# Kernel tuning notes

Hardware: AMD Instinct MI355X
Metric: run time of the kernel (lower is better)

Reference implementation:

```python
import jax, jax.numpy as jnp
import numpy as np

PI = float(np.pi)


def _conv2d(x, w, b, pad):
    out = jax.lax.conv_general_dilated(x, w, (1, 1), ((pad, pad), (pad, pad)),
                                       dimension_numbers=('NCHW', 'OIHW', 'NCHW'))
    return out + b[None, :, None, None]


def _group_norm(x, gamma, beta, groups, eps=1e-5):
    B, C, h, w = x.shape
    xg = x.reshape(B, groups, C // groups, h, w)
    mu = xg.mean(axis=(2, 3, 4), keepdims=True)
    var = xg.var(axis=(2, 3, 4), keepdims=True)
    xn = ((xg - mu) / jnp.sqrt(var + eps)).reshape(B, C, h, w)
    return xn * gamma[None, :, None, None] + beta[None, :, None, None]


def _l2n(x, eps=1e-12):
    return x / jnp.maximum(jnp.linalg.norm(x, axis=1, keepdims=True), eps)


def _dense_sift(x):
    # kornia DenseSIFTDescriptor defaults: 8 ang bins, 4x4 spatial bins,
    # spatial_bin_size=4, rootsift=True, clipval=0.2, stride=1, padding=1
    eps = 1e-10
    NA = 8
    # 'diff' spatial gradient with replicate padding, normalized (/2)
    xp = jnp.pad(x, ((0, 0), (0, 0), (1, 1), (1, 1)), mode='edge')
    gx = (xp[:, :, 1:-1, 2:] - xp[:, :, 1:-1, :-2]) * 0.5
    gy = (xp[:, :, 2:, 1:-1] - xp[:, :, :-2, 1:-1]) * 0.5
    mag = jnp.sqrt(gx * gx + gy * gy + eps)[:, 0]           # [B,H,W]
    ori = jnp.arctan2(gy, gx + eps)[:, 0] + 2.0 * PI
    o_big = NA * ori / (2.0 * PI)
    bo0f = jnp.floor(o_big)
    wo1_ = o_big - bo0f
    wo0 = (1.0 - wo1_) * mag
    wo1 = wo1_ * mag
    bo0 = bo0f.astype(jnp.int32) % NA
    bo1 = (bo0 + 1) % NA
    bins = jnp.arange(NA).reshape(1, NA, 1, 1)
    ang = ((bo0[:, None] == bins).astype(x.dtype) * wo0[:, None]
           + (bo1[:, None] == bins).astype(x.dtype) * wo1[:, None])  # [B,8,H,W]
    # SIFT pooling kernel ksize=4 (triangle weights), conv pad=2 -> H+1,W+1
    xc2 = np.array([0.5, 1.5, 1.5, 0.5], np.float32)
    pool1 = np.outer(xc2, xc2) / 4.0
    pk = jnp.asarray(np.tile(pool1[None, None], (NA, 1, 1, 1)))  # depthwise [8,1,4,4]
    pooled = jax.lax.conv_general_dilated(ang, pk, (1, 1), ((2, 2), (2, 2)),
                dimension_numbers=('NCHW', 'OIHW', 'NCHW'), feature_group_count=NA)
    # identity reshape conv: 128 = 8 ang * 4*4 spatial bins, pad=1 -> back to H,W
    rk = jnp.asarray(np.eye(128, dtype=np.float32).reshape(128, NA, 4, 4))
    out = jax.lax.conv_general_dilated(pooled, rk, (1, 1), ((1, 1), (1, 1)),
                dimension_numbers=('NCHW', 'OIHW', 'NCHW'))
    out = jnp.clip(_l2n(out), 0.0, 0.2)
    out = _l2n(out)
    l1 = jnp.maximum(jnp.sum(jnp.abs(out), axis=1, keepdims=True), 1e-12)
    return jnp.sqrt(out / l1 + eps)  # rootsift


def _joint_bilateral(x, guide, ksize=5, sigma_color=0.1, sigma_space=1.5):
    pad = ksize // 2
    ax = np.arange(ksize, dtype=np.float32) - ksize // 2
    g1 = np.exp(-ax ** 2 / (2.0 * sigma_space ** 2))
    g1 = g1 / g1.sum()
    sk = np.outer(g1, g1)  # normalized 5x5 gaussian space kernel
    xp = jnp.pad(x, ((0, 0), (0, 0), (pad, pad), (pad, pad)), mode='reflect')
    gp = jnp.pad(guide, ((0, 0), (0, 0), (pad, pad), (pad, pad)), mode='reflect')
    h, w = x.shape[2], x.shape[3]
    inv = -0.5 / (sigma_color ** 2)
    num = jnp.zeros_like(x)
    den = jnp.zeros((x.shape[0], 1, h, w), x.dtype)
    for dy in range(ksize):           # fixed 5x5 tap loop, accumulated in-place
        for dx in range(ksize):
            gs = gp[:, :, dy:dy + h, dx:dx + w]
            cd = jnp.sum(jnp.abs(gs - guide), axis=1, keepdims=True) ** 2  # l1 squared
            wgt = sk[dy, dx] * jnp.exp(inv * cd)
            num = num + wgt * xp[:, :, dy:dy + h, dx:dx + w]
            den = den + wgt
    return num / den


def _forward(x, gt, w1, b1, g1w, g1b, w2, b2, g2w, g2b, w3, b3, g3w, g3b,
             w4, b4, g4w, g4b, w5, b5):
    orig = x
    f = _dense_sift(x)
    f = jax.nn.relu(_group_norm(_conv2d(f, w1, b1, 2), g1w, g1b, 8))
    f = jax.nn.relu(_group_norm(_conv2d(f, w2, b2, 1), g2w, g2b, 8))
    f = jax.nn.relu(_group_norm(_conv2d(f, w3, b3, 1), g3w, g3b, 4))
    f = jax.nn.relu(_group_norm(_conv2d(f, w4, b4, 1), g4w, g4b, 4))
    f = _conv2d(f, w5, b5, 1)
    # rgb_to_yuv(gt)[:, 1:] as guidance
    r, g, b = gt[:, 0], gt[:, 1], gt[:, 2]
    u = -0.147 * r - 0.289 * g + 0.436 * b
    v = 0.615 * r - 0.515 * g - 0.100 * b
    guide = jnp.stack([u, v], axis=1)
    f = _joint_bilateral(f, guide)

    def _rescale(c, lo, hi):
        c = (c - c.min()) / (c.max() - c.min() + 1e-6)  # global min/max over B,H,W
        c = jnp.clip(c, 0.0, 1.0)
        return c * (hi - lo) + lo

    U = _rescale(f[:, 0], -0.436, 0.436)
    V = _rescale(f[:, 1], -0.615, 0.615)
    Y = orig[:, 0]
    R = Y + 1.14 * V
    G = Y - 0.396 * U - 0.581 * V
    B = Y + 2.029 * U
    return jnp.stack([R, G, B], axis=1)


def setup_inputs() -> dict:
    key = jax.random.key(0)
    ks = jax.random.split(key, 16)
    B = 4
    d = {
        'x': jax.random.uniform(ks[0], (B, 1, 270, 512), jnp.float32),
        'gt': jax.random.uniform(ks[1], (B, 3, 270, 512), jnp.float32),
        'w1': jax.random.normal(ks[2], (64, 128, 5, 5), jnp.float32) * 0.02,
        'b1': jnp.zeros((64,), jnp.float32),
        'g1w': jnp.ones((64,), jnp.float32), 'g1b': jnp.zeros((64,), jnp.float32),
        'w2': jax.random.normal(ks[3], (32, 64, 3, 3), jnp.float32) * 0.04,
        'b2': jnp.zeros((32,), jnp.float32),
        'g2w': jnp.ones((32,), jnp.float32), 'g2b': jnp.zeros((32,), jnp.float32),
        'w3': jax.random.normal(ks[4], (16, 32, 3, 3), jnp.float32) * 0.05,
        'b3': jnp.zeros((16,), jnp.float32),
        'g3w': jnp.ones((16,), jnp.float32), 'g3b': jnp.zeros((16,), jnp.float32),
        'w4': jax.random.normal(ks[5], (8, 16, 3, 3), jnp.float32) * 0.08,
        'b4': jnp.zeros((8,), jnp.float32),
        'g4w': jnp.ones((8,), jnp.float32), 'g4b': jnp.zeros((8,), jnp.float32),
        'w5': jax.random.normal(ks[6], (2, 8, 3, 3), jnp.float32) * 0.1,
        'b5': jnp.zeros((2,), jnp.float32),
    }
    return d


def reference(x, gt, w1, b1, g1w, g1b, w2, b2, g2w, g2b, w3, b3, g3w, g3b,
              w4, b4, g4w, g4b, w5, b5):
    return _forward(x, gt, w1, b1, g1w, g1b, w2, b2, g2w, g2b, w3, b3, g3w, g3b,
                    w4, b4, g4w, g4b, w5, b5)
```

## Files before the change

kernel.cpp:

```cpp
#include <hip/hip_runtime.h>

constexpr int NB  = 4;
constexpr int IH  = 270;
constexpr int IW  = 512;
constexpr int NPIX = IH * IW;
constexpr int PH  = 271;
constexpr int PW  = 513;
constexpr float TWO_PI_F = 6.28318530717958647692f;

typedef short  bf16x8 __attribute__((ext_vector_type(8)));
typedef float floatx4 __attribute__((ext_vector_type(4)));

__device__ inline short f2bf(float x) {
  union { float f; unsigned u; } un; un.f = x;
  unsigned r = un.u + 0x7fff + ((un.u >> 16) & 1);
  return (short)(r >> 16);
}
__device__ inline unsigned fkey(float f) {
  unsigned u = __float_as_uint(f);
  return (u & 0x80000000u) ? ~u : (u | 0x80000000u);
}
__device__ inline float funkey(unsigned k) {
  unsigned u = (k & 0x80000000u) ? (k ^ 0x80000000u) : ~k;
  return __uint_as_float(u);
}
__device__ inline void gn_coef_thread(const float* __restrict__ stats,
                                      const float* __restrict__ gamma,
                                      const float* __restrict__ beta,
                                      float* cA, float* cB, int C, int chper, int b) {
  int c = threadIdx.x;
  if (c < C) {
    int g0 = (c / chper) * chper;
    float S = 0.f, S2 = 0.f;
    for (int k = 0; k < chper; k++) {
      S  += stats[(b * C + g0 + k) * 2];
      S2 += stats[(b * C + g0 + k) * 2 + 1];
    }
    double Nd = (double)chper * NPIX;
    double mu = (double)S / Nd;
    double var = (double)S2 / Nd - mu * mu;
    double rstd = 1.0 / sqrt(var + 1e-5);
    float A = (float)rstd * gamma[c];
    cA[c] = A;
    cB[c] = beta[c] - (float)mu * A;
  }
}

__device__ inline void mfma_pack_one(const float* __restrict__ w, short* __restrict__ wB,
                                     int i, int CO, int CI, int KK, int CHUNKS) {
  int j = i & 7, l = (i >> 3) & 63, f = i >> 9;
  int t = f % KK; int fc = f / KK; int cc = fc % CHUNKS; int g = fc / CHUNKS;
  int ci = cc * 32 + ((l >> 4) << 3) + j;
  int co = g * 16 + (l & 15);
  float v = (ci < CI && co < CO) ? w[((size_t)co * CI + ci) * KK + t] : 0.f;
  wB[i] = f2bf(v);
}
__device__ inline void repack_one(const float* __restrict__ w, float* __restrict__ wT,
                                  int i, int CO, int CI, int KK) {
  int o = i / (CI * KK);
  int r = i % (CI * KK);
  int ci = r / KK, kk = r % KK;
  wT[(kk * CI + ci) * CO + o] = w[i];
}
__global__ __launch_bounds__(256) void prep_kernel(
    const float* __restrict__ w1, const float* __restrict__ w2,
    const float* __restrict__ w3, const float* __restrict__ w4,
    const float* __restrict__ w5,
    short* __restrict__ w1B, short* __restrict__ w2B, short* __restrict__ w3B,
    float* __restrict__ w4T, float* __restrict__ w5T) {
  constexpr int N1 = 4 * 4 * 25 * 512;
  constexpr int N2 = 2 * 2 * 9 * 512;
  constexpr int N3 = 1 * 1 * 9 * 512;
  constexpr int N4 = 8 * 16 * 9;
  constexpr int N5 = 2 * 8 * 9;
  int i = blockIdx.x * 256 + threadIdx.x;
  if (i < N1) { mfma_pack_one(w1, w1B, i, 64, 128, 25, 4); return; }
  i -= N1;
  if (i < N2) { mfma_pack_one(w2, w2B, i, 32, 64, 9, 2); return; }
  i -= N2;
  if (i < N3) { mfma_pack_one(w3, w3B, i, 16, 32, 9, 1); return; }
  i -= N3;
  if (i < N4) { repack_one(w4, w4T, i, 8, 16, 9); return; }
  i -= N4;
  if (i < N5) { repack_one(w5, w5T, i, 2, 8, 9); return; }
}

__global__ __launch_bounds__(256) void pooled_kernel(
    const float* __restrict__ x, float* __restrict__ pooled) {
  const int b = blockIdx.z;
  const int px0 = blockIdx.x * 16, py0 = blockIdx.y * 16;
  __shared__ float wo0s[19][19];
  __shared__ float wo1s[19][19];
  __shared__ int   bo0s[19][19];
  const float* xb = x + (size_t)b * NPIX;

  for (int t = threadIdx.x; t < 19 * 19; t += 256) {
    int r = t / 19, c = t % 19;
    int gy = py0 - 2 + r, gx = px0 - 2 + c;
    float w0 = 0.f, w1v = 0.f; int b0 = 0;
    if (gy >= 0 && gy < IH && gx >= 0 && gx < IW) {
      int xm = gx > 0 ? gx - 1 : 0, xp = gx < IW - 1 ? gx + 1 : IW - 1;
      int ym = gy > 0 ? gy - 1 : 0, yp = gy < IH - 1 ? gy + 1 : IH - 1;
      float gxv = (xb[gy * IW + xp] - xb[gy * IW + xm]) * 0.5f;
      float gyv = (xb[yp * IW + gx] - xb[ym * IW + gx]) * 0.5f;
      float mag = sqrtf(gxv * gxv + gyv * gyv + 1e-10f);
      float ori = atan2f(gyv, gxv + 1e-10f) + TWO_PI_F;
      float obig = ori * (8.0f / TWO_PI_F);
      float bf = floorf(obig);
      float w1_ = obig - bf;
      w0  = (1.0f - w1_) * mag;
      w1v = w1_ * mag;
      b0  = ((int)bf) & 7;
    }
    wo0s[r][c] = w0; wo1s[r][c] = w1v; bo0s[r][c] = b0;
  }
  __syncthreads();

  const int t = threadIdx.x;
  const int lx = t % 16, ly = t / 16;
  const int py = py0 + ly, px = px0 + lx;
  if (py >= PH || px >= PW) return;

  const float pwt[4] = {0.25f, 0.75f, 0.75f, 0.25f};
  float acc[8] = {0, 0, 0, 0, 0, 0, 0, 0};
  for (int i = 0; i < 4; i++) {
    for (int j = 0; j < 4; j++) {
      int r = ly + i, c = lx + j;
      float w0 = wo0s[r][c], w1v = wo1s[r][c];
      int b0 = bo0s[r][c];
      int b1i = (b0 + 1) & 7;
      float pw = pwt[i] * pwt[j];
      #pragma unroll
      for (int a = 0; a < 8; a++) {
        float add = (a == b0 ? w0 : 0.f) + (a == b1i ? w1v : 0.f);
        acc[a] = fmaf(pw, add, acc[a]);
      }
    }
  }
  float* pb = pooled + (size_t)b * 8 * PH * PW;
  #pragma unroll
  for (int a = 0; a < 8; a++) pb[((size_t)a * PH + py) * PW + px] = acc[a];
}

__global__ __launch_bounds__(256) void sift_scalars_kernel(
    const float* __restrict__ pooled, float* __restrict__ s1g) {
  const int b = blockIdx.z;
  const int x0 = blockIdx.x * 16, y0 = blockIdx.y * 16;
  __shared__ float pt[8][19][19];
  const float* pb = pooled + (size_t)b * 8 * PH * PW;
  for (int t = threadIdx.x; t < 8 * 19 * 19; t += 256) {
    int a = t / 361, rc = t % 361, r = rc / 19, c = rc % 19;
    int gy = y0 - 1 + r, gx = x0 - 1 + c;
    float v = 0.f;
    if (gy >= 0 && gy < PH && gx >= 0 && gx < PW) v = pb[((size_t)a * PH + gy) * PW + gx];
    pt[a][r][c] = v;
  }
  __syncthreads();
  const int t = threadIdx.x;
  const int lx = t % 16, ly = t / 16;
  const int y = y0 + ly, x = x0 + lx;
  if (y >= IH) return;

  float sum2 = 0.f;
  for (int c = 0; c < 128; c++) {
    int a = c >> 4, i = (c >> 2) & 3, j = c & 3;
    float p = pt[a][ly + i][lx + j];
    sum2 = fmaf(p, p, sum2);
  }
  float s1 = 1.0f / fmaxf(sqrtf(sum2), 1e-12f);
  float st2 = 0.f, st = 0.f;
  for (int c = 0; c < 128; c++) {
    int a = c >> 4, i = (c >> 2) & 3, j = c & 3;
    float p = pt[a][ly + i][lx + j];
    float tv = fminf(p * s1, 0.2f);
    st2 = fmaf(tv, tv, st2);
    st += tv;
  }
  float s2 = 1.0f / fmaxf(sqrtf(st2), 1e-12f);
  float l1 = fmaxf(s2 * st, 1e-12f);
  float g = s2 / l1;
  float* o = s1g + (size_t)b * 2 * NPIX;
  o[y * IW + x] = s1;
  o[NPIX + y * IW + x] = g;
}

__global__ __launch_bounds__(256, 2) void conv1_mfma_kernel(
    const float* __restrict__ pooled, const float* __restrict__ s1g,
    const short* __restrict__ w1B, const float* __restrict__ bias,
    float* __restrict__ out, float* __restrict__ stats) {
  const int b = blockIdx.z;
  const int x0 = blockIdx.x * 16, y0 = blockIdx.y * 16;
  __shared__ __align__(16) char smem_raw[39440];
  short* desc = (short*)smem_raw;
  float* sc   = (float*)(smem_raw + 32000);
  float* pt   = (float*)(smem_raw + 35208);
  float* cout = (float*)smem_raw;

  const int tid = threadIdx.x;
  const int wave = tid >> 6, lane = tid & 63;
  const int quad = lane >> 4, lm = lane & 15;

  const float* pb = pooled + (size_t)b * 8 * PH * PW;
  const float* sb = s1g + (size_t)b * 2 * NPIX;
  for (int t = tid; t < 400; t += 256) {
    int r = t / 20, c = t % 20;
    int gy = y0 - 2 + r, gx = x0 - 2 + c;
    float a0 = 0.f, a1 = 0.f;
    if (gy >= 0 && gy < IH && gx >= 0 && gx < IW) {
      a0 = sb[gy * IW + gx];
      a1 = sb[NPIX + gy * IW + gx];
    }
    sc[t] = a0; sc[400 + t] = a1;
  }
  for (int t = tid; t < 1058; t += 256) {
    int pl = t / 529, rc = t % 529, r = rc / 23, c = rc % 23;
    int gy = y0 - 3 + r, gx = x0 - 3 + c;
    float v = 0.f;
    if (gy >= 0 && gy < PH && gx >= 0 && gx < PW) v = pb[((size_t)pl * PH + gy) * PW + gx];
    pt[t] = v;
  }

  floatx4 acc[4][4];
  #pragma unroll
  for (int n = 0; n < 4; n++)
    #pragma unroll
    for (int i = 0; i < 4; i++) acc[n][i] = (floatx4){0.f, 0.f, 0.f, 0.f};

  for (int cc = 0; cc < 4; cc++) {
    __syncthreads();
    for (int v = tid; v < 3200; v += 256) {
      int pos = v % 400, cg = v / 400;
      int r = pos / 20, c = pos % 20;
      int gy = y0 - 2 + r, gx = x0 - 2 + c;
      bool ok = (gy >= 0 && gy < IH && gx >= 0 && gx < IW);
      int al = cg >> 2;
      int ii = cg & 3;
      float s1v = sc[pos], gv = sc[400 + pos];
      const float* prow = pt + al * 529 + (r + ii) * 23 + c;
      unsigned short o4[4];
      #pragma unroll
      for (int q = 0; q < 4; q++) {
        float p = prow[q];
        float val = ok ? sqrtf(fminf(p * s1v, 0.2f) * gv + 1e-10f) : 0.f;
        o4[q] = (unsigned short)f2bf(val);
      }
      uint2 pk;
      pk.x = (unsigned)o4[0] | ((unsigned)o4[1] << 16);
      pk.y = (unsigned)o4[2] | ((unsigned)o4[3] << 16);
      *(uint2*)(desc + pos * 40 + cg * 4) = pk;
    }
    __syncthreads();

    if (cc < 3) {
      for (int t = tid; t < 1058; t += 256) {
        int pl = t / 529, rc = t % 529, r = rc / 23, c = rc % 23;
        int gy = y0 - 3 + r, gx = x0 - 3 + c;
        float v = 0.f;
        if (gy >= 0 && gy < PH && gx >= 0 && gx < PW)
          v = pb[((size_t)(2 * (cc + 1) + pl) * PH + gy) * PW + gx];
        pt[t] = v;
      }
    }

    #pragma unroll
    for (int ky = 0; ky < 5; ky++) {
      #pragma unroll
      for (int kx = 0; kx < 5; kx++) {
        bf16x8 bfr[4];
        #pragma unroll
        for (int n = 0; n < 4; n++) {
          int f = (n * 4 + cc) * 25 + ky * 5 + kx;
          bfr[n] = *(const bf16x8*)(w1B + ((size_t)f << 9) + (lane << 3));
        }
        bf16x8 av[4];
        #pragma unroll
        for (int i = 0; i < 4; i++) {
          int mt = wave * 4 + i;
          av[i] = *(const bf16x8*)(desc + ((mt + ky) * 20 + lm + kx) * 40 + quad * 8);
        }
        #pragma unroll
        for (int n = 0; n < 4; n++)
          #pragma unroll
          for (int i = 0; i < 4; i++)
            acc[n][i] = __builtin_amdgcn_mfma_f32_16x16x32_bf16(av[i], bfr[n], acc[n][i], 0, 0, 0);
      }
    }
  }

  float* ob = out + (size_t)b * 64 * NPIX;
  for (int h = 0; h < 2; h++) {
    __syncthreads();
    #pragma unroll
    for (int nn = 0; nn < 2; nn++)
      #pragma unroll
      for (int i = 0; i < 4; i++)
        #pragma unroll
        for (int r = 0; r < 4; r++)
          cout[(nn * 16 + lm) * 261 + (wave * 4 + i) * 16 + quad * 4 + r] = acc[h * 2 + nn][i][r];
    __syncthreads();
    for (int v = tid; v < 8192; v += 256) {
      int col = v >> 8, px = v & 255;
      int y = y0 + (px >> 4), x = x0 + (px & 15);
      if (y < IH)
        ob[(size_t)(h * 32 + col) * NPIX + y * IW + x] = cout[col * 261 + px] + bias[h * 32 + col];
    }
    int col = tid >> 3, seg = tid & 7;
    int co = h * 32 + col;
    float bv = bias[co];
    float sum = 0.f, sq = 0.f;
    #pragma unroll
    for (int rr = 0; rr < 2; rr++) {
      int row = seg * 2 + rr;
      if (y0 + row < IH) {
        #pragma unroll
        for (int k = 0; k < 16; k++) {
          float vv = cout[col * 261 + row * 16 + k] + bv;
          sum += vv; sq += vv * vv;
        }
      }
    }
    sum += __shfl_down(sum, 4); sq += __shfl_down(sq, 4);
    sum += __shfl_down(sum, 2); sq += __shfl_down(sq, 2);
    sum += __shfl_down(sum, 1); sq += __shfl_down(sq, 1);
    if ((tid & 7) == 0) {
      atomicAdd(&stats[(b * 64 + co) * 2], sum);
      atomicAdd(&stats[(b * 64 + co) * 2 + 1], sq);
    }
  }
}

template <int CI, int CO, int CHPER, bool STATS>
__global__ __launch_bounds__(256) void convk3_mfma_kernel(
    const float* __restrict__ xin, const short* __restrict__ wB,
    const float* __restrict__ bias, const float* __restrict__ statsIn,
    const float* __restrict__ gamma, const float* __restrict__ beta,
    float* __restrict__ statsOut, float* __restrict__ out) {
  constexpr int CHUNKS = CI / 32;
  constexpr int G = CO / 16;
  constexpr int MPW = 2 * G;
  constexpr int CIS = CI + 8;
  constexpr int TILE_B = 180 * CIS * 2;
  constexpr int COUT_B = CO * 133 * 4;
  constexpr int UNION_B = TILE_B > COUT_B ? TILE_B : COUT_B;
  __shared__ __align__(16) char sm[UNION_B + CI * 8];
  short* tile = (short*)sm;
  float* cout = (float*)sm;
  float* cA = (float*)(sm + UNION_B);
  float* cB = cA + CI;

  const int b = blockIdx.z;
  const int x0 = blockIdx.x * 16, y0 = blockIdx.y * 8;
  const int tid = threadIdx.x;
  const int wave = tid >> 6, lane = tid & 63;
  const int quad = lane >> 4, lm = lane & 15;
  const int n = wave % G, mh = wave / G;

  gn_coef_thread(statsIn, gamma, beta, cA, cB, CI, CHPER, b);
  __syncthreads();

  const float* xb = xin + (size_t)b * CI * NPIX;
  for (int v = tid; v < (CI / 2) * 180; v += 256) {
    int cp = v / 180, pos = v % 180;
    int r = pos / 18, c = pos % 18;
    int gy = y0 - 1 + r, gx = x0 - 1 + c;
    float v0 = 0.f, v1 = 0.f;
    if (gy >= 0 && gy < IH && gx >= 0 && gx < IW) {
      v0 = fmaxf(fmaf(xb[(size_t)(2 * cp) * NPIX + gy * IW + gx], cA[2 * cp], cB[2 * cp]), 0.f);
      v1 = fmaxf(fmaf(xb[(size_t)(2 * cp + 1) * NPIX + gy * IW + gx], cA[2 * cp + 1], cB[2 * cp + 1]), 0.f);
    }
    unsigned pk = (unsigned)(unsigned short)f2bf(v0) |
                  ((unsigned)(unsigned short)f2bf(v1) << 16);
    *(unsigned*)(tile + pos * CIS + 2 * cp) = pk;
  }
  __syncthreads();

  floatx4 acc[MPW];
  #pragma unroll
  for (int i = 0; i < MPW; i++) acc[i] = (floatx4){0.f, 0.f, 0.f, 0.f};

  #pragma unroll
  for (int cc = 0; cc < CHUNKS; cc++) {
    #pragma unroll
    for (int ky = 0; ky < 3; ky++) {
      #pragma unroll
      for (int kx = 0; kx < 3; kx++) {
        int f = (n * CHUNKS + cc) * 9 + ky * 3 + kx;
        bf16x8 bfr = *(const bf16x8*)(wB + ((size_t)f << 9) + (lane << 3));
        #pragma unroll
        for (int i = 0; i < MPW; i++) {
          int mt = mh * MPW + i;
          bf16x8 av = *(const bf16x8*)(tile + ((mt + ky) * 18 + lm + kx) * CIS + cc * 32 + quad * 8);
          acc[i] = __builtin_amdgcn_mfma_f32_16x16x32_bf16(av, bfr, acc[i], 0, 0, 0);
        }
      }
    }
  }
  __syncthreads();
  #pragma unroll
  for (int i = 0; i < MPW; i++) {
    #pragma unroll
    for (int r = 0; r < 4; r++) {
      int pixel = (mh * MPW + i) * 16 + quad * 4 + r;
      cout[(n * 16 + lm) * 133 + pixel] = acc[i][r];
    }
  }
  __syncthreads();
  float* ob = out + (size_t)b * CO * NPIX;
  for (int v = tid; v < CO * 128; v += 256) {
    int co = v >> 7, px = v & 127;
    int y = y0 + (px >> 4), x = x0 + (px & 15);
    if (y < IH) ob[(size_t)co * NPIX + y * IW + x] = cout[co * 133 + px] + bias[co];
  }
  if (STATS) {
    constexpr int TPC = 256 / CO;
    constexpr int PXT = 128 / TPC;
    int col = tid / TPC, seg = tid % TPC;
    float bv = bias[col];
    float sum = 0.f, sq = 0.f;
    #pragma unroll
    for (int k = 0; k < PXT; k++) {
      int p = seg * PXT + k;
      if (y0 + (p >> 4) < IH) {
        float vv = cout[col * 133 + p] + bv;
        sum += vv; sq += vv * vv;
      }
    }
    #pragma unroll
    for (int off = TPC / 2; off > 0; off >>= 1) {
      sum += __shfl_down(sum, off);
      sq  += __shfl_down(sq, off);
    }
    if (seg == 0) {
      atomicAdd(&statsOut[(b * CO + col) * 2], sum);
      atomicAdd(&statsOut[(b * CO + col) * 2 + 1], sq);
    }
  }
}

template <int CI, int CO, int CHPER, bool STATS>
__global__ __launch_bounds__(256) void convs_kernel(
    const float* __restrict__ xin, const float* __restrict__ wT,
    const float* __restrict__ bias, const float* __restrict__ statsIn,
    const float* __restrict__ gamma, const float* __restrict__ beta,
    float* __restrict__ statsOut, float* __restrict__ out) {
  constexpr int OPT = CO / 2;
  const int b = blockIdx.z;
  const int x0 = blockIdx.x * 16, y0 = blockIdx.y * 8;
  __shared__ float tile[CI * 180];
  __shared__ float cA[CI], cB[CI];
  __shared__ float ssum[CO], ssq[CO];
  gn_coef_thread(statsIn, gamma, beta, cA, cB, CI, CHPER, b);
  if (STATS && threadIdx.x < CO) { ssum[threadIdx.x] = 0.f; ssq[threadIdx.x] = 0.f; }
  __syncthreads();
  const float* xb = xin + (size_t)b * CI * NPIX;
  for (int t = threadIdx.x; t < CI * 180; t += 256) {
    int ci = t / 180, rc = t % 180, r = rc / 18, c = rc % 18;
    int gy = y0 - 1 + r, gx = x0 - 1 + c;
    float v = 0.f;
    if (gy >= 0 && gy < IH && gx >= 0 && gx < IW)
      v = fmaxf(fmaf(xb[(size_t)ci * NPIX + gy * IW + gx], cA[ci], cB[ci]), 0.f);
    tile[t] = v;
  }
  __syncthreads();
  const int t = threadIdx.x;
  const int px = t & 127, og = t >> 7;
  const int pyy = px >> 4, pxx = px & 15;
  const int oc0 = og * OPT;
  const int y = y0 + pyy, x = x0 + pxx;
  float acc[OPT] = {};
  for (int ky = 0; ky < 3; ky++) {
    for (int kx = 0; kx < 3; kx++) {
      const float* wrow = wT + (size_t)((ky * 3 + kx) * CI) * CO + oc0;
      for (int ci = 0; ci < CI; ci++) {
        float v = tile[ci * 180 + (pyy + ky) * 18 + pxx + kx];
        #pragma unroll
        for (int o = 0; o < OPT; o++) acc[o] = fmaf(v, wrow[ci * CO + o], acc[o]);
      }
    }
  }
  if (y < IH) {
    float* ob = out + (size_t)b * CO * NPIX;
    #pragma unroll
    for (int o = 0; o < OPT; o++) {
      float vv = acc[o] + bias[oc0 + o];
      ob[(size_t)(oc0 + o) * NPIX + y * IW + x] = vv;
      if (STATS) {
        atomicAdd(&ssum[oc0 + o], vv);
        atomicAdd(&ssq[oc0 + o], vv * vv);
      }
    }
  }
  if (STATS) {
    __syncthreads();
    if (threadIdx.x < CO) {
      atomicAdd(&statsOut[(b * CO + threadIdx.x) * 2], ssum[threadIdx.x]);
      atomicAdd(&statsOut[(b * CO + threadIdx.x) * 2 + 1], ssq[threadIdx.x]);
    }
  }
}

__global__ __launch_bounds__(256) void bilateral_kernel(
    const float* __restrict__ f, const float* __restrict__ gt,
    float* __restrict__ out, unsigned* __restrict__ mmbits) {
  const int b = blockIdx.z;
  const int x0 = blockIdx.x * 16, y0 = blockIdx.y * 16;
  __shared__ float gu[20][20], gv[20][20], f0s[20][20], f1s[20][20];
  __shared__ float red[4][4];
  const float* gtb = gt + (size_t)b * 3 * NPIX;
  const float* fb = f + (size_t)b * 2 * NPIX;
  for (int t = threadIdx.x; t < 400; t += 256) {
    int r = t / 20, c = t % 20;
    int gy = y0 - 2 + r, gx = x0 - 2 + c;
    if (gy < 0) gy = -gy;
    if (gy > IH - 1) gy = 2 * (IH - 1) - gy;
    if (gx < 0) gx = -gx;
    if (gx > IW - 1) gx = 2 * (IW - 1) - gx;
    int p = gy * IW + gx;
    float rr = gtb[p], gg = gtb[NPIX + p], bb = gtb[2 * NPIX + p];
    gu[r][c]  = -0.147f * rr - 0.289f * gg + 0.436f * bb;
    gv[r][c]  =  0.615f * rr - 0.515f * gg - 0.100f * bb;
    f0s[r][c] = fb[p];
    f1s[r][c] = fb[NPIX + p];
  }
  __syncthreads();
  const int t = threadIdx.x;
  const int lx = t % 16, ly = t / 16;
  const int y = y0 + ly, x = x0 + lx;
  const bool valid = (y < IH);

  float o0 = 0.f, o1 = 0.f;
  if (valid) {
    float g1v[5];
    float s = 0.f;
    #pragma unroll
    for (int k = 0; k < 5; k++) {
      float a = (float)(k - 2);
      g1v[k] = expf(-a * a / 4.5f);
      s += g1v[k];
    }
    #pragma unroll
    for (int k = 0; k < 5; k++) g1v[k] /= s;
    float cu = gu[ly + 2][lx + 2], cv = gv[ly + 2][lx + 2];
    float num0 = 0.f, num1 = 0.f, den = 0.f;
    #pragma unroll
    for (int dy = 0; dy < 5; dy++) {
      #pragma unroll
      for (int dx = 0; dx < 5; dx++) {
        float du = fabsf(gu[ly + dy][lx + dx] - cu) + fabsf(gv[ly + dy][lx + dx] - cv);
        float wgt = g1v[dy] * g1v[dx] * expf(-50.0f * du * du);
        num0 = fmaf(wgt, f0s[ly + dy][lx + dx], num0);
        num1 = fmaf(wgt, f1s[ly + dy][lx + dx], num1);
        den += wgt;
      }
    }
    o0 = num0 / den; o1 = num1 / den;
    float* ob = out + (size_t)b * 2 * NPIX;
    ob[y * IW + x] = o0;
    ob[NPIX + y * IW + x] = o1;
  }
  float mn0 = valid ? o0 : 1e30f,  mx0 = valid ? o0 : -1e30f;
  float mn1 = valid ? o1 : 1e30f,  mx1 = valid ? o1 : -1e30f;
  #pragma unroll
  for (int off = 32; off > 0; off >>= 1) {
    mn0 = fminf(mn0, __shfl_xor(mn0, off));
    mx0 = fmaxf(mx0, __shfl_xor(mx0, off));
    mn1 = fminf(mn1, __shfl_xor(mn1, off));
    mx1 = fmaxf(mx1, __shfl_xor(mx1, off));
  }
  if ((t & 63) == 0) {
    red[t >> 6][0] = mn0; red[t >> 6][1] = mx0;
    red[t >> 6][2] = mn1; red[t >> 6][3] = mx1;
  }
  __syncthreads();
  if (t == 0) {
    for (int w = 1; w < 4; w++) {
      red[0][0] = fminf(red[0][0], red[w][0]);
      red[0][1] = fmaxf(red[0][1], red[w][1]);
      red[0][2] = fminf(red[0][2], red[w][2]);
      red[0][3] = fmaxf(red[0][3], red[w][3]);
    }
    atomicMax(&mmbits[0], fkey(red[0][1]));
    atomicMax(&mmbits[1], fkey(red[0][3]));
    atomicMin(&mmbits[2], fkey(red[0][0]));
    atomicMin(&mmbits[3], fkey(red[0][2]));
  }
}

__global__ __launch_bounds__(256) void final_kernel(
    const float* __restrict__ bil, const float* __restrict__ x,
    const unsigned* __restrict__ mmbits, float* __restrict__ out) {
  int i = blockIdx.x * 256 + threadIdx.x;
  if (i >= NB * NPIX) return;
  float mx0 = funkey(mmbits[0]), mx1 = funkey(mmbits[1]);
  float mn0 = funkey(mmbits[2]), mn1 = funkey(mmbits[3]);
  int b = i / NPIX, p = i % NPIX;
  float f0 = bil[(size_t)b * 2 * NPIX + p];
  float f1 = bil[(size_t)b * 2 * NPIX + NPIX + p];
  float U = (f0 - mn0) / (mx0 - mn0 + 1e-6f);
  U = fminf(fmaxf(U, 0.f), 1.f) * 0.872f - 0.436f;
  float V = (f1 - mn1) / (mx1 - mn1 + 1e-6f);
  V = fminf(fmaxf(V, 0.f), 1.f) * 1.23f - 0.615f;
  float Y = x[(size_t)b * NPIX + p];
  float* ob = out + (size_t)b * 3 * NPIX;
  ob[p]            = Y + 1.14f * V;
  ob[NPIX + p]     = Y - 0.396f * U - 0.581f * V;
  ob[2 * NPIX + p] = Y + 2.029f * U;
}

extern "C" void kernel_launch(void* const* d_in, const int* in_sizes, int n_in,
                              void* d_out, int out_size, void* d_ws, size_t ws_size,
                              hipStream_t stream) {
  const float* x   = (const float*)d_in[0];
  const float* gt  = (const float*)d_in[1];
  const float* w1  = (const float*)d_in[2];
  const float* b1  = (const float*)d_in[3];
  const float* g1w = (const float*)d_in[4];
  const float* g1b = (const float*)d_in[5];
  const float* w2  = (const float*)d_in[6];
  const float* b2  = (const float*)d_in[7];
  const float* g2w = (const float*)d_in[8];
  const float* g2b = (const float*)d_in[9];
  const float* w3  = (const float*)d_in[10];
  const float* b3  = (const float*)d_in[11];
  const float* g3w = (const float*)d_in[12];
  const float* g3b = (const float*)d_in[13];
  const float* w4  = (const float*)d_in[14];
  const float* b4  = (const float*)d_in[15];
  const float* g4w = (const float*)d_in[16];
  const float* g4b = (const float*)d_in[17];
  const float* w5  = (const float*)d_in[18];
  const float* b5  = (const float*)d_in[19];
  float* out = (float*)d_out;

  char* ws = (char*)d_ws;
  float* stats1 = (float*)ws;
  float* stats2 = stats1 + 512;
  float* stats3 = stats2 + 256;
  float* stats4 = stats3 + 128;
  unsigned* mmbits = (unsigned*)(ws + 12288);
  float* fbase  = (float*)(ws + 16384);
  size_t off = 0;
  float* pooled = fbase + off; off += 4452864;
  float* s1g    = fbase + off; off += 1105920;
  short* w1B    = (short*)(fbase + off); off += 102400;
  short* w2B    = (short*)(fbase + off); off += 9216;
  short* w3B    = (short*)(fbase + off); off += 2304;
  float* w4T    = fbase + off; off += 1152;
  float* w5T    = fbase + off; off += 256;
  float* bufA   = fbase + off; off += 35389440;
  float* bufB   = fbase + off; off += 17694720;
  float* c5     = pooled;
  float* bilat  = pooled + 1105920;

  hipMemsetAsync(ws, 0, 12304, stream);
  hipMemsetAsync(ws + 12296, 0xFF, 8, stream);

  prep_kernel<<<896, 256, 0, stream>>>(w1, w2, w3, w4, w5, w1B, w2B, w3B, w4T, w5T);

  pooled_kernel<<<dim3(33, 17, NB), 256, 0, stream>>>(x, pooled);
  sift_scalars_kernel<<<dim3(32, 17, NB), 256, 0, stream>>>(pooled, s1g);
  conv1_mfma_kernel<<<dim3(32, 17, NB), 256, 0, stream>>>(pooled, s1g, w1B, b1, bufA, stats1);

  convk3_mfma_kernel<64, 32, 8, true><<<dim3(32, 34, NB), 256, 0, stream>>>(
      bufA, w2B, b2, stats1, g1w, g1b, stats2, bufB);

  convk3_mfma_kernel<32, 16, 4, true><<<dim3(32, 34, NB), 256, 0, stream>>>(
      bufB, w3B, b3, stats2, g2w, g2b, stats3, bufA);

  convs_kernel<16, 8, 4, true><<<dim3(32, 34, NB), 256, 0, stream>>>(
      bufA, w4T, b4, stats3, g3w, g3b, stats4, bufB);

  convs_kernel<8, 2, 2, false><<<dim3(32, 34, NB), 256, 0, stream>>>(
      bufB, w5T, b5, stats4, g4w, g4b, nullptr, c5);

  bilateral_kernel<<<dim3(32, 17, NB), 256, 0, stream>>>(c5, gt, bilat, mmbits);
  final_kernel<<<(NB * NPIX + 255) / 256, 256, 0, stream>>>(bilat, x, mmbits, out);

  (void)in_sizes; (void)n_in; (void)out_size; (void)ws_size;
}
```

Before: 1.415 ms.

## Fuse SIFT pooling and scalars into descriptor kernel; store intermediates as bf16

Merges the pooled and sift_scalars kernels into one kernel that computes gradients, pooling, normalization scalars and the final rootSIFT descriptor in shared memory, then writes a bf16 descriptor laid out for the MFMA conv1 loader. conv1 now just copies descriptor vectors instead of recomputing them per tile. All intermediate conv activations are also stored as bf16 instead of fp32, which halves activation traffic. The costs are a larger descriptor buffer (128 bf16 channels per pixel), extra rounding of activations before GroupNorm statistics, and a workspace layout that overlaps buffers.

```diff
diff --git a/kernel.cpp b/kernel.cpp
--- a/kernel.cpp
+++ b/kernel.cpp
@@ -11,10 +11,13 @@
 typedef short  bf16x8 __attribute__((ext_vector_type(8)));
 typedef float floatx4 __attribute__((ext_vector_type(4)));
 
-__device__ inline short f2bf(float x) {
+__device__ inline unsigned short f2bf(float x) {
   union { float f; unsigned u; } un; un.f = x;
   unsigned r = un.u + 0x7fff + ((un.u >> 16) & 1);
-  return (short)(r >> 16);
+  return (unsigned short)(r >> 16);
+}
+__device__ inline float bf2f(unsigned short u) {
+  union { unsigned u; float f; } x; x.u = ((unsigned)u) << 16; return x.f;
 }
 __device__ inline unsigned fkey(float f) {
   unsigned u = __float_as_uint(f);
@@ -53,7 +56,7 @@
   int ci = cc * 32 + ((l >> 4) << 3) + j;
   int co = g * 16 + (l & 15);
   float v = (ci < CI && co < CO) ? w[((size_t)co * CI + ci) * KK + t] : 0.f;
-  wB[i] = f2bf(v);
+  wB[i] = (short)f2bf(v);
 }
 __device__ inline void repack_one(const float* __restrict__ w, float* __restrict__ wT,
                                   int i, int CO, int CI, int KK) {
@@ -85,24 +88,33 @@
   if (i < N5) { repack_one(w5, w5T, i, 2, 8, 9); return; }
 }
 
-__global__ __launch_bounds__(256) void pooled_kernel(
-    const float* __restrict__ x, float* __restrict__ pooled) {
+__global__ __launch_bounds__(256) void sift_desc_kernel(
+    const float* __restrict__ x, short* __restrict__ descg) {
   const int b = blockIdx.z;
-  const int px0 = blockIdx.x * 16, py0 = blockIdx.y * 16;
-  __shared__ float wo0s[19][19];
-  __shared__ float wo1s[19][19];
-  __shared__ int   bo0s[19][19];
+  const int x0 = blockIdx.x * 16, y0 = blockIdx.y * 16;
+  __shared__ float xs[24][25];
+  __shared__ float wo0[22][23], wo1[22][23];
+  __shared__ int   bo0[22][23];
+  __shared__ float pooled[8][19][20];
+  __shared__ float s1s[256], gs[256];
+  const int tid = threadIdx.x;
   const float* xb = x + (size_t)b * NPIX;
 
-  for (int t = threadIdx.x; t < 19 * 19; t += 256) {
-    int r = t / 19, c = t % 19;
-    int gy = py0 - 2 + r, gx = px0 - 2 + c;
+  for (int t = tid; t < 576; t += 256) {
+    int r = t / 24, c = t % 24;
+    int gy = min(max(y0 - 4 + r, 0), IH - 1);
+    int gx = min(max(x0 - 4 + c, 0), IW - 1);
+    xs[r][c] = xb[gy * IW + gx];
+  }
+  __syncthreads();
+
+  for (int t = tid; t < 484; t += 256) {
+    int r = t / 22, c = t % 22;
+    int gy = y0 - 3 + r, gx = x0 - 3 + c;
     float w0 = 0.f, w1v = 0.f; int b0 = 0;
     if (gy >= 0 && gy < IH && gx >= 0 && gx < IW) {
-      int xm = gx > 0 ? gx - 1 : 0, xp = gx < IW - 1 ? gx + 1 : IW - 1;
-      int ym = gy > 0 ? gy - 1 : 0, yp = gy < IH - 1 ? gy + 1 : IH - 1;
-      float gxv = (xb[gy * IW + xp] - xb[gy * IW + xm]) * 0.5f;
-      float gyv = (xb[yp * IW + gx] - xb[ym * IW + gx]) * 0.5f;
+      float gxv = (xs[r + 1][c + 2] - xs[r + 1][c]) * 0.5f;
+      float gyv = (xs[r + 2][c + 1] - xs[r][c + 1]) * 0.5f;
       float mag = sqrtf(gxv * gxv + gyv * gyv + 1e-10f);
       float ori = atan2f(gyv, gxv + 1e-10f) + TWO_PI_F;
       float obig = ori * (8.0f / TWO_PI_F);
@@ -112,114 +124,105 @@
       w1v = w1_ * mag;
       b0  = ((int)bf) & 7;
     }
-    wo0s[r][c] = w0; wo1s[r][c] = w1v; bo0s[r][c] = b0;
-  }
-  __syncthreads();
-
-  const int t = threadIdx.x;
-  const int lx = t % 16, ly = t / 16;
-  const int py = py0 + ly, px = px0 + lx;
-  if (py >= PH || px >= PW) return;
+    wo0[r][c] = w0; wo1[r][c] = w1v; bo0[r][c] = b0;
+  }
+  __syncthreads();
 
   const float pwt[4] = {0.25f, 0.75f, 0.75f, 0.25f};
-  float acc[8] = {0, 0, 0, 0, 0, 0, 0, 0};
-  for (int i = 0; i < 4; i++) {
-    for (int j = 0; j < 4; j++) {
-      int r = ly + i, c = lx + j;
-      float w0 = wo0s[r][c], w1v = wo1s[r][c];
-      int b0 = bo0s[r][c];
-      int b1i = (b0 + 1) & 7;
-      float pw = pwt[i] * pwt[j];
+  for (int t = tid; t < 361; t += 256) {
+    int pr = t / 19, pc = t % 19;
+    int py = y0 - 1 + pr, px = x0 - 1 + pc;
+    float acc[8] = {0, 0, 0, 0, 0, 0, 0, 0};
+    if (py >= 0 && py < PH && px >= 0 && px < PW) {
       #pragma unroll
-      for (int a = 0; a < 8; a++) {
-        float add = (a == b0 ? w0 : 0.f) + (a == b1i ? w1v : 0.f);
-        acc[a] = fmaf(pw, add, acc[a]);
-      }
-    }
-  }
-  float* pb = pooled + (size_t)b * 8 * PH * PW;
-  #pragma unroll
-  for (int a = 0; a < 8; a++) pb[((size_t)a * PH + py) * PW + px] = acc[a];
-}
-
-__global__ __launch_bounds__(256) void sift_scalars_kernel(
-    const float* __restrict__ pooled, float* __restrict__ s1g) {
+      for (int i = 0; i < 4; i++) {
+        #pragma unroll
+        for (int j = 0; j < 4; j++) {
+          float w0 = wo0[pr + i][pc + j], w1v = wo1[pr + i][pc + j];
+          int b0 = bo0[pr + i][pc + j];
+          int b1i = (b0 + 1) & 7;
+          float pw = pwt[i] * pwt[j];
+          #pragma unroll
+          for (int a = 0; a < 8; a++) {
+            float add = (a == b0 ? w0 : 0.f) + (a == b1i ? w1v : 0.f);
+            acc[a] = fmaf(pw, add, acc[a]);
+          }
+        }
+      }
+    }
+    #pragma unroll
+    for (int a = 0; a < 8; a++) pooled[a][pr][pc] = acc[a];
+  }
+  __syncthreads();
+
+  {
+    int py = tid >> 4, px = tid & 15;
+    int y = y0 + py;
+    float s1 = 0.f, g = 0.f;
+    if (y < IH) {
+      float sum2 = 0.f;
+      for (int c = 0; c < 128; c++) {
+        int a = c >> 4, i = (c >> 2) & 3, j = c & 3;
+        float p = pooled[a][py + i][px + j];
+        sum2 = fmaf(p, p, sum2);
+      }
+      s1 = 1.0f / fmaxf(sqrtf(sum2), 1e-12f);
+      float st2 = 0.f, st = 0.f;
+      for (int c = 0; c < 128; c++) {
+        int a = c >> 4, i = (c >> 2) & 3, j = c & 3;
+        float p = pooled[a][py + i][px + j];
+        float tv = fminf(p * s1, 0.2f);
+        st2 = fmaf(tv, tv, st2);
+        st += tv;
+      }
+      float s2 = 1.0f / fmaxf(sqrtf(st2), 1e-12f);
+      float l1 = fmaxf(s2 * st, 1e-12f);
+      g = s2 / l1;
+    }
+    s1s[tid] = s1; gs[tid] = g;
+  }
+  __syncthreads();
+
+  for (int k = 0; k < 16; k++) {
+    int gidx = k * 256 + tid;
+    int cc = gidx >> 10, pix = (gidx >> 2) & 255, sub = gidx & 3;
+    int py = pix >> 4, px = pix & 15;
+    int y = y0 + py;
+    if (y >= IH) continue;
+    float s1v = s1s[pix], gv = gs[pix];
+    int a = cc * 2 + (sub >> 1);
+    unsigned short v8[8];
+    #pragma unroll
+    for (int jj = 0; jj < 8; jj++) {
+      int i = (sub * 2 + (jj >> 2)) & 3;
+      int j = jj & 3;
+      float p = pooled[a][py + i][px + j];
+      v8[jj] = f2bf(sqrtf(fminf(p * s1v, 0.2f) * gv + 1e-10f));
+    }
+    uint4 pk;
+    pk.x = (unsigned)v8[0] | ((unsigned)v8[1] << 16);
+    pk.y = (unsigned)v8[2] | ((unsigned)v8[3] << 16);
+    pk.z = (unsigned)v8[4] | ((unsigned)v8[5] << 16);
+    pk.w = (unsigned)v8[6] | ((unsigned)v8[7] << 16);
+    size_t base = ((size_t)(b * 4 + cc) * NPIX + (size_t)y * IW + (x0 + px)) * 32 + sub * 8;
+    *(uint4*)(descg + base) = pk;
+  }
+}
+
+__global__ __launch_bounds__(256, 2) void conv1_mfma_kernel(
+    const short* __restrict__ descg, const short* __restrict__ w1B,
+    const float* __restrict__ bias, unsigned short* __restrict__ out,
+    float* __restrict__ stats) {
   const int b = blockIdx.z;
   const int x0 = blockIdx.x * 16, y0 = blockIdx.y * 16;
-  __shared__ float pt[8][19][19];
-  const float* pb = pooled + (size_t)b * 8 * PH * PW;
-  for (int t = threadIdx.x; t < 8 * 19 * 19; t += 256) {
-    int a = t / 361, rc = t % 361, r = rc / 19, c = rc % 19;
-    int gy = y0 - 1 + r, gx = x0 - 1 + c;
-    float v = 0.f;
-    if (gy >= 0 && gy < PH && gx >= 0 && gx < PW) v = pb[((size_t)a * PH + gy) * PW + gx];
-    pt[a][r][c] = v;
-  }
-  __syncthreads();
-  const int t = threadIdx.x;
-  const int lx = t % 16, ly = t / 16;
-  const int y = y0 + ly, x = x0 + lx;
-  if (y >= IH) return;
-
-  float sum2 = 0.f;
-  for (int c = 0; c < 128; c++) {
-    int a = c >> 4, i = (c >> 2) & 3, j = c & 3;
-    float p = pt[a][ly + i][lx + j];
-    sum2 = fmaf(p, p, sum2);
-  }
-  float s1 = 1.0f / fmaxf(sqrtf(sum2), 1e-12f);
-  float st2 = 0.f, st = 0.f;
-  for (int c = 0; c < 128; c++) {
-    int a = c >> 4, i = (c >> 2) & 3, j = c & 3;
-    float p = pt[a][ly + i][lx + j];
-    float tv = fminf(p * s1, 0.2f);
-    st2 = fmaf(tv, tv, st2);
-    st += tv;
-  }
-  float s2 = 1.0f / fmaxf(sqrtf(st2), 1e-12f);
-  float l1 = fmaxf(s2 * st, 1e-12f);
-  float g = s2 / l1;
-  float* o = s1g + (size_t)b * 2 * NPIX;
-  o[y * IW + x] = s1;
-  o[NPIX + y * IW + x] = g;
-}
-
-__global__ __launch_bounds__(256, 2) void conv1_mfma_kernel(
-    const float* __restrict__ pooled, const float* __restrict__ s1g,
-    const short* __restrict__ w1B, const float* __restrict__ bias,
-    float* __restrict__ out, float* __restrict__ stats) {
-  const int b = blockIdx.z;
-  const int x0 = blockIdx.x * 16, y0 = blockIdx.y * 16;
-  __shared__ __align__(16) char smem_raw[39440];
+  __shared__ __align__(16) char smem_raw[33408];
   short* desc = (short*)smem_raw;
-  float* sc   = (float*)(smem_raw + 32000);
-  float* pt   = (float*)(smem_raw + 35208);
   float* cout = (float*)smem_raw;
 
   const int tid = threadIdx.x;
   const int wave = tid >> 6, lane = tid & 63;
   const int quad = lane >> 4, lm = lane & 15;
 
-  const float* pb = pooled + (size_t)b * 8 * PH * PW;
-  const float* sb = s1g + (size_t)b * 2 * NPIX;
-  for (int t = tid; t < 400; t += 256) {
-    int r = t / 20, c = t % 20;
-    int gy = y0 - 2 + r, gx = x0 - 2 + c;
-    float a0 = 0.f, a1 = 0.f;
-    if (gy >= 0 && gy < IH && gx >= 0 && gx < IW) {
-      a0 = sb[gy * IW + gx];
-      a1 = sb[NPIX + gy * IW + gx];
-    }
-    sc[t] = a0; sc[400 + t] = a1;
-  }
-  for (int t = tid; t < 1058; t += 256) {
-    int pl = t / 529, rc = t % 529, r = rc / 23, c = rc % 23;
-    int gy = y0 - 3 + r, gx = x0 - 3 + c;
-    float v = 0.f;
-    if (gy >= 0 && gy < PH && gx >= 0 && gx < PW) v = pb[((size_t)pl * PH + gy) * PW + gx];
-    pt[t] = v;
-  }
-
   floatx4 acc[4][4];
   #pragma unroll
   for (int n = 0; n < 4; n++)
@@ -228,39 +231,17 @@
 
   for (int cc = 0; cc < 4; cc++) {
     __syncthreads();
-    for (int v = tid; v < 3200; v += 256) {
-      int pos = v % 400, cg = v / 400;
+    const short* dg = descg + (size_t)(b * 4 + cc) * NPIX * 32;
+    for (int u = tid; u < 1600; u += 256) {
+      int pos = u >> 2, sub = u & 3;
       int r = pos / 20, c = pos % 20;
       int gy = y0 - 2 + r, gx = x0 - 2 + c;
-      bool ok = (gy >= 0 && gy < IH && gx >= 0 && gx < IW);
-      int al = cg >> 2;
-      int ii = cg & 3;
-      float s1v = sc[pos], gv = sc[400 + pos];
-      const float* prow = pt + al * 529 + (r + ii) * 23 + c;
-      unsigned short o4[4];
-      #pragma unroll
-      for (int q = 0; q < 4; q++) {
-        float p = prow[q];
-        float val = ok ? sqrtf(fminf(p * s1v, 0.2f) * gv + 1e-10f) : 0.f;
-        o4[q] = (unsigned short)f2bf(val);
-      }
-      uint2 pk;
-      pk.x = (unsigned)o4[0] | ((unsigned)o4[1] << 16);
-      pk.y = (unsigned)o4[2] | ((unsigned)o4[3] << 16);
-      *(uint2*)(desc + pos * 40 + cg * 4) = pk;
+      uint4 val = {0u, 0u, 0u, 0u};
+      if (gy >= 0 && gy < IH && gx >= 0 && gx < IW)
+        val = *(const uint4*)(dg + ((size_t)gy * IW + gx) * 32 + sub * 8);
+      *(uint4*)(desc + pos * 40 + sub * 8) = val;
     }
     __syncthreads();
-
-    if (cc < 3) {
-      for (int t = tid; t < 1058; t += 256) {
-        int pl = t / 529, rc = t % 529, r = rc / 23, c = rc % 23;
-        int gy = y0 - 3 + r, gx = x0 - 3 + c;
-        float v = 0.f;
-        if (gy >= 0 && gy < PH && gx >= 0 && gx < PW)
-          v = pb[((size_t)(2 * (cc + 1) + pl) * PH + gy) * PW + gx];
-        pt[t] = v;
-      }
-    }
 
     #pragma unroll
     for (int ky = 0; ky < 5; ky++) {
@@ -287,7 +268,7 @@
     }
   }
 
-  float* ob = out + (size_t)b * 64 * NPIX;
+  unsigned short* ob = out + (size_t)b * 64 * NPIX;
   for (int h = 0; h < 2; h++) {
     __syncthreads();
     #pragma unroll
@@ -302,7 +283,7 @@
       int col = v >> 8, px = v & 255;
       int y = y0 + (px >> 4), x = x0 + (px & 15);
       if (y < IH)
-        ob[(size_t)(h * 32 + col) * NPIX + y * IW + x] = cout[col * 261 + px] + bias[h * 32 + col];
+        ob[(size_t)(h * 32 + col) * NPIX + y * IW + x] = f2bf(cout[col * 261 + px] + bias[h * 32 + col]);
     }
     int col = tid >> 3, seg = tid & 7;
     int co = h * 32 + col;
@@ -331,10 +312,10 @@
 
 template <int CI, int CO, int CHPER, bool STATS>
 __global__ __launch_bounds__(256) void convk3_mfma_kernel(
-    const float* __restrict__ xin, const short* __restrict__ wB,
+    const unsigned short* __restrict__ xin, const short* __restrict__ wB,
     const float* __restrict__ bias, const float* __restrict__ statsIn,
     const float* __restrict__ gamma, const float* __restrict__ beta,
-    float* __restrict__ statsOut, float* __restrict__ out) {
+    float* __restrict__ statsOut, unsigned short* __restrict__ out) {
   constexpr int CHUNKS = CI / 32;
   constexpr int G = CO / 16;
   constexpr int MPW = 2 * G;
@@ -358,18 +339,17 @@
   gn_coef_thread(statsIn, gamma, beta, cA, cB, CI, CHPER, b);
   __syncthreads();
 
-  const float* xb = xin + (size_t)b * CI * NPIX;
+  const unsigned short* xb = xin + (size_t)b * CI * NPIX;
   for (int v = tid; v < (CI / 2) * 180; v += 256) {
     int cp = v / 180, pos = v % 180;
     int r = pos / 18, c = pos % 18;
     int gy = y0 - 1 + r, gx = x0 - 1 + c;
     float v0 = 0.f, v1 = 0.f;
     if (gy >= 0 && gy < IH && gx >= 0 && gx < IW) {
-      v0 = fmaxf(fmaf(xb[(size_t)(2 * cp) * NPIX + gy * IW + gx], cA[2 * cp], cB[2 * cp]), 0.f);
-      v1 = fmaxf(fmaf(xb[(size_t)(2 * cp + 1) * NPIX + gy * IW + gx], cA[2 * cp + 1], cB[2 * cp + 1]), 0.f);
-    }
-    unsigned pk = (unsigned)(unsigned short)f2bf(v0) |
-                  ((unsigned)(unsigned short)f2bf(v1) << 16);
+      v0 = fmaxf(fmaf(bf2f(xb[(size_t)(2 * cp) * NPIX + gy * IW + gx]), cA[2 * cp], cB[2 * cp]), 0.f);
+      v1 = fmaxf(fmaf(bf2f(xb[(size_t)(2 * cp + 1) * NPIX + gy * IW + gx]), cA[2 * cp + 1], cB[2 * cp + 1]), 0.f);
+    }
+    unsigned pk = (unsigned)f2bf(v0) | ((unsigned)f2bf(v1) << 16);
     *(unsigned*)(tile + pos * CIS + 2 * cp) = pk;
   }
   __syncthreads();
@@ -405,11 +385,11 @@
     }
   }
   __syncthreads();
-  float* ob = out + (size_t)b * CO * NPIX;
+  unsigned short* ob = out + (size_t)b * CO * NPIX;
   for (int v = tid; v < CO * 128; v += 256) {
     int co = v >> 7, px = v & 127;
     int y = y0 + (px >> 4), x = x0 + (px & 15);
-    if (y < IH) ob[(size_t)co * NPIX + y * IW + x] = cout[co * 133 + px] + bias[co];
+    if (y < IH) ob[(size_t)co * NPIX + y * IW + x] = f2bf(cout[co * 133 + px] + bias[co]);
   }
   if (STATS) {
     constexpr int TPC = 256 / CO;
@@ -437,12 +417,12 @@
   }
 }
 
-template <int CI, int CO, int CHPER, bool STATS>
+template <int CI, int CO, int CHPER, bool STATS, bool OUT_BF16>
 __global__ __launch_bounds__(256) void convs_kernel(
-    const float* __restrict__ xin, const float* __restrict__ wT,
+    const unsigned short* __restrict__ xin, const float* __restrict__ wT,
     const float* __restrict__ bias, const float* __restrict__ statsIn,
     const float* __restrict__ gamma, const float* __restrict__ beta,
-    float* __restrict__ statsOut, float* __restrict__ out) {
+    float* __restrict__ statsOut, void* __restrict__ outv) {
   constexpr int OPT = CO / 2;
   const int b = blockIdx.z;
   const int x0 = blockIdx.x * 16, y0 = blockIdx.y * 8;
@@ -452,13 +432,13 @@
   gn_coef_thread(statsIn, gamma, beta, cA, cB, CI, CHPER, b);
   if (STATS && threadIdx.x < CO) { ssum[threadIdx.x] = 0.f; ssq[threadIdx.x] = 0.f; }
   __syncthreads();
-  const float* xb = xin + (size_t)b * CI * NPIX;
+  const unsigned short* xb = xin + (size_t)b * CI * NPIX;
   for (int t = threadIdx.x; t < CI * 180; t += 256) {
     int ci = t / 180, rc = t % 180, r = rc / 18, c = rc % 18;
     int gy = y0 - 1 + r, gx = x0 - 1 + c;
     float v = 0.f;
     if (gy >= 0 && gy < IH && gx >= 0 && gx < IW)
-      v = fmaxf(fmaf(xb[(size_t)ci * NPIX + gy * IW + gx], cA[ci], cB[ci]), 0.f);
+      v = fmaxf(fmaf(bf2f(xb[(size_t)ci * NPIX + gy * IW + gx]), cA[ci], cB[ci]), 0.f);
     tile[t] = v;
   }
   __syncthreads();
@@ -479,11 +459,16 @@
     }
   }
   if (y < IH) {
-    float* ob = out + (size_t)b * CO * NPIX;
     #pragma unroll
     for (int o = 0; o < OPT; o++) {
       float vv = acc[o] + bias[oc0 + o];
-      ob[(size_t)(oc0 + o) * NPIX + y * IW + x] = vv;
+      if (OUT_BF16) {
+        unsigned short* ob = (unsigned short*)outv + (size_t)b * CO * NPIX;
+        ob[(size_t)(oc0 + o) * NPIX + y * IW + x] = f2bf(vv);
+      } else {
+        float* ob = (float*)outv + (size_t)b * CO * NPIX;
+        ob[(size_t)(oc0 + o) * NPIX + y * IW + x] = vv;
+      }
       if (STATS) {
         atomicAdd(&ssum[oc0 + o], vv);
         atomicAdd(&ssq[oc0 + o], vv * vv);
@@ -638,40 +623,39 @@
   float* stats3 = stats2 + 256;
   float* stats4 = stats3 + 128;
   unsigned* mmbits = (unsigned*)(ws + 12288);
-  float* fbase  = (float*)(ws + 16384);
-  size_t off = 0;
-  float* pooled = fbase + off; off += 4452864;
-  float* s1g    = fbase + off; off += 1105920;
-  short* w1B    = (short*)(fbase + off); off += 102400;
-  short* w2B    = (short*)(fbase + off); off += 9216;
-  short* w3B    = (short*)(fbase + off); off += 2304;
-  float* w4T    = fbase + off; off += 1152;
-  float* w5T    = fbase + off; off += 256;
-  float* bufA   = fbase + off; off += 35389440;
-  float* bufB   = fbase + off; off += 17694720;
-  float* c5     = pooled;
-  float* bilat  = pooled + 1105920;
+  char* base = ws + 16384;
+  short* descg = (short*)base;
+  size_t descg_shorts = (size_t)NB * 4 * NPIX * 32;
+  unsigned short* bufB_h = (unsigned short*)base;
+  float* c5    = (float*)(base + 36000000);
+  float* bilat = (float*)(base + 41000000);
+  short* w1B = descg + descg_shorts;
+  short* w2B = w1B + 204800;
+  short* w3B = w2B + 18432;
+  float* w4T = (float*)(w3B + 4608);
+  float* w5T = w4T + 1152;
+  unsigned short* bufA_h = (unsigned short*)(w5T + 144);
 
   hipMemsetAsync(ws, 0, 12304, stream);
   hipMemsetAsync(ws + 12296, 0xFF, 8, stream);
 
   prep_kernel<<<896, 256, 0, stream>>>(w1, w2, w3, w4, w5, w1B, w2B, w3B, w4T, w5T);
 
-  pooled_kernel<<<dim3(33, 17, NB), 256, 0, stream>>>(x, pooled);
-  sift_scalars_kernel<<<dim3(32, 17, NB), 256, 0, stream>>>(pooled, s1g);
-  conv1_mfma_kernel<<<dim3(32, 17, NB), 256, 0, stream>>>(pooled, s1g, w1B, b1, bufA, stats1);
+  sift_desc_kernel<<<dim3(32, 17, NB), 256, 0, stream>>>(x, descg);
+
+  conv1_mfma_kernel<<<dim3(32, 17, NB), 256, 0, stream>>>(descg, w1B, b1, bufA_h, stats1);
 
   convk3_mfma_kernel<64, 32, 8, true><<<dim3(32, 34, NB), 256, 0, stream>>>(
-      bufA, w2B, b2, stats1, g1w, g1b, stats2, bufB);
+      bufA_h, w2B, b2, stats1, g1w, g1b, stats2, bufB_h);
 
   convk3_mfma_kernel<32, 16, 4, true><<<dim3(32, 34, NB), 256, 0, stream>>>(
-      bufB, w3B, b3, stats2, g2w, g2b, stats3, bufA);
-
-  convs_kernel<16, 8, 4, true><<<dim3(32, 34, NB), 256, 0, stream>>>(
-      bufA, w4T, b4, stats3, g3w, g3b, stats4, bufB);
-
-  convs_kernel<8, 2, 2, false><<<dim3(32, 34, NB), 256, 0, stream>>>(
-      bufB, w5T, b5, stats4, g4w, g4b, nullptr, c5);
+      bufB_h, w3B, b3, stats2, g2w, g2b, stats3, bufA_h);
+
+  convs_kernel<16, 8, 4, true, true><<<dim3(32, 34, NB), 256, 0, stream>>>(
+      bufA_h, w4T, b4, stats3, g3w, g3b, stats4, bufB_h);
+
+  convs_kernel<8, 2, 2, false, false><<<dim3(32, 34, NB), 256, 0, stream>>>(
+      bufB_h, w5T, b5, stats4, g4w, g4b, nullptr, c5);
 
   bilateral_kernel<<<dim3(32, 17, NB), 256, 0, stream>>>(c5, gt, bilat, mmbits);
   final_kernel<<<(NB * NPIX + 255) / 256, 256, 0, stream>>>(bilat, x, mmbits, out);
```

Result: faster. 1.310 ms (-7.4%).
